# Kernel tuning notes

Measured on AMD Instinct MI355X. Metric: run time of the kernel, lower is better.

## Reference

```python
import jax, jax.numpy as jnp
import numpy as np

NUM_DIRECTIONS = 100  # matches init_kwargs
N_POINTS = 200000


def setup_inputs() -> dict:
    key = jax.random.key(0)
    k1, k2 = jax.random.split(key)
    X = jax.random.normal(k1, (N_POINTS, 2), dtype=jnp.float32)
    Y = jax.random.normal(k2, (N_POINTS, 2), dtype=jnp.float32)
    return {"X": X, "Y": Y}


def _lines():
    # thetas = linspace(-pi/2, pi/2, K+1)[:-1]; lines[i] = (cos t_i, sin t_i)
    thetas = jnp.linspace(-np.pi / 2, np.pi / 2, NUM_DIRECTIONS + 1)[:-1]
    L = jnp.stack([jnp.cos(thetas), jnp.sin(thetas)], axis=1).astype(jnp.float32)  # [K, 2]
    return L


def reference(X, Y):
    # X, Y: [N, 2], [M, 2] persistence diagrams (birth, death)
    L = _lines()                                   # [K, 2]
    inv_norm = 1.0 / jnp.sum(L * L, axis=1)        # [K] (== 1 analytically, kept for fidelity)
    diag = jnp.array([0.5, 0.5], dtype=jnp.float32)

    # diagonal projections of each diagram: sum(point) * [0.5, 0.5]
    X_diag = jnp.sum(X, axis=1, keepdims=True) * diag  # [N, 2]
    Y_diag = jnp.sum(Y, axis=1, keepdims=True) * diag  # [M, 2]

    # batched line projections: replaces per-point dot-product loops
    proj_X = (X @ L.T) * inv_norm                  # [N, K]
    proj_Y = (Y @ L.T) * inv_norm                  # [M, K]
    proj_Xd = (X_diag @ L.T) * inv_norm            # [N, K]
    proj_Yd = (Y_diag @ L.T) * inv_norm            # [M, K]

    # 1D EMD per direction: sort both multisets, sum |diff|
    A = jnp.sort(jnp.concatenate([proj_X, proj_Yd], axis=0), axis=0)  # [N+M, K]
    B = jnp.sort(jnp.concatenate([proj_Y, proj_Xd], axis=0), axis=0)  # [N+M, K]

    total_cost = jnp.sum(jnp.abs(A - B)) / NUM_DIRECTIONS
    return total_cost
```

## Files before the change

### kernel.cpp

```cpp
#include <hip/hip_runtime.h>

#define KDIR 100
#define TILE 4096
#define NPASS 3
#define MBLK 512
#define MOUT 4096
#define MPT 8

struct TrueT  { static constexpr bool value = true; };
struct FalseT { static constexpr bool value = false; };

__device__ __forceinline__ unsigned encodeF(float f) {
  unsigned u = __float_as_uint(f);
  return u ^ ((u >> 31) ? 0xFFFFFFFFu : 0x80000000u);
}
__device__ __forceinline__ float decodeU(unsigned u) {
  return __uint_as_float(u ^ ((u >> 31) ? 0x80000000u : 0xFFFFFFFFu));
}

__global__ void k_table(float* tbl, double* part, int nSlots) {
  int k = threadIdx.x;
  const double PI = 3.14159265358979323846;
  if (k < KDIR) {
    double th = -PI * 0.5 + (double)k * (PI / (double)KDIR);
    float c = (float)cos(th), s = (float)sin(th);
    float invn = 1.0f / (c * c + s * s);
    tbl[k] = c; tbl[128 + k] = s; tbl[256 + k] = (c + s) * invn; tbl[384 + k] = invn;
  }
  if (k == 100) { tbl[100] = 0.5f; tbl[228] = 0.5f; tbl[484] = 1.0f; }
  for (int i = k; i < nSlots; i += 256) part[i] = 0.0;
}

__device__ __forceinline__ void buildTile(const float* __restrict__ p0, int nItems,
                                          float ck, float sk, float inv,
                                          unsigned* __restrict__ d0, unsigned* h, int tid) {
  if (nItems == TILE) {
    const float4* p4 = (const float4*)p0;
    uint2* o2 = (uint2*)d0;
#pragma unroll
    for (int i = 0; i < 8; ++i) {
      float4 v = p4[i * 256 + tid];
      unsigned ua = encodeF((v.x * ck + v.y * sk) * inv);
      unsigned ub = encodeF((v.z * ck + v.w * sk) * inv);
      o2[i * 256 + tid] = make_uint2(ua, ub);
      atomicAdd(&h[(ua >> 8) & 255u], 1u);
      atomicAdd(&h[(ub >> 8) & 255u], 1u);
    }
  } else {
    for (int j = tid; j < nItems; j += 256) {
      float x = p0[2 * j], y = p0[2 * j + 1];
      unsigned u = encodeF((x * ck + y * sk) * inv);
      d0[j] = u;
      atomicAdd(&h[(u >> 8) & 255u], 1u);
    }
  }
}

__global__ __launch_bounds__(256) void k_buildAll(const float* __restrict__ X,
                                                  const float* __restrict__ Y, int n,
                                                  const float* __restrict__ tbl,
                                                  unsigned* __restrict__ dst,
                                                  unsigned* __restrict__ counts, int T) {
  __shared__ unsigned h[256];
  int tid = threadIdx.x;
  h[tid] = 0;
  __syncthreads();
  int dir = blockIdx.y;
  int k = (dir < KDIR) ? dir : (dir < 2 * KDIR ? dir - KDIR : KDIR);
  const float* P = (dir < KDIR || dir == 2 * KDIR) ? X : Y;
  float ck = tbl[k], sk = tbl[128 + k], inv = tbl[384 + k];
  int tile = blockIdx.x;
  int start = tile * TILE;
  int nItems = min(TILE, n - start);
  buildTile(P + 2 * (size_t)start, nItems, ck, sk, inv,
            dst + (size_t)dir * n + start, h, tid);
  __syncthreads();
  counts[((size_t)dir * 256 + tid) * T + tile] = h[tid];
}

__global__ __launch_bounds__(256) void k_build(const float* __restrict__ P, int n, int kIdx,
                                               const float* __restrict__ tbl,
                                               unsigned* __restrict__ dst,
                                               unsigned* __restrict__ counts, int T, int seg0) {
  __shared__ unsigned h[256];
  int tid = threadIdx.x;
  h[tid] = 0;
  __syncthreads();
  int dir = blockIdx.y;
  int k = kIdx + dir;
  float ck = tbl[k], sk = tbl[128 + k], inv = tbl[384 + k];
  int tile = blockIdx.x;
  int start = tile * TILE;
  int nItems = min(TILE, n - start);
  buildTile(P + 2 * (size_t)start, nItems, ck, sk, inv,
            dst + (size_t)dir * n + start, h, tid);
  __syncthreads();
  counts[((size_t)(seg0 + dir) * 256 + tid) * T + tile] = h[tid];
}

__global__ __launch_bounds__(256) void k_hist8(const unsigned* __restrict__ keys,
                                               int L, int T, int shift,
                                               unsigned* __restrict__ counts) {
  __shared__ unsigned h[4][256];
  int tid = threadIdx.x;
  int w = tid >> 6;
  for (int i = tid; i < 4 * 256; i += 256) ((unsigned*)h)[i] = 0;
  __syncthreads();
  int seg = blockIdx.y, tile = blockIdx.x;
  const unsigned* base = keys + (size_t)seg * L + (size_t)tile * TILE;
  int nItems = min(TILE, L - tile * TILE);
  if (nItems == TILE) {
    const uint4* b4 = (const uint4*)base;
#pragma unroll
    for (int i = 0; i < 4; ++i) {
      uint4 v = b4[i * 256 + tid];
      atomicAdd(&h[w][(v.x >> shift) & 255u], 1u);
      atomicAdd(&h[w][(v.y >> shift) & 255u], 1u);
      atomicAdd(&h[w][(v.z >> shift) & 255u], 1u);
      atomicAdd(&h[w][(v.w >> shift) & 255u], 1u);
    }
  } else {
    for (int i = tid; i < nItems; i += 256)
      atomicAdd(&h[w][(base[i] >> shift) & 255u], 1u);
  }
  __syncthreads();
  counts[((size_t)seg * 256 + tid) * T + tile] =
      h[0][tid] + h[1][tid] + h[2][tid] + h[3][tid];
}

__global__ __launch_bounds__(256) void k_scanSeg(unsigned* __restrict__ counts, int T) {
  __shared__ unsigned tot[256];
  unsigned* c = counts + (size_t)blockIdx.x * 256 * T;
  int tid = threadIdx.x;
  int base = tid * T;
  unsigned sum = 0;
  for (int i = 0; i < T; ++i) sum += c[base + i];
  tot[tid] = sum;
  __syncthreads();
  for (int ofs = 1; ofs < 256; ofs <<= 1) {
    unsigned t = (tid >= ofs) ? tot[tid - ofs] : 0u;
    __syncthreads();
    tot[tid] += t;
    __syncthreads();
  }
  unsigned run = tot[tid] - sum;
  for (int i = 0; i < T; ++i) {
    unsigned v = c[base + i];
    c[base + i] = run;
    run += v;
  }
}

__global__ __launch_bounds__(256) void k_scatter8(const unsigned* __restrict__ src,
                                                  unsigned* __restrict__ dst,
                                                  int L, int T, int shift,
                                                  const unsigned* __restrict__ counts,
                                                  unsigned* __restrict__ nextCounts,
                                                  int shift2) {
  __shared__ unsigned runG[4][4][256];
  __shared__ unsigned diffD[256];
  __shared__ unsigned wsum[4];
  int tid = threadIdx.x;
  int lane = tid & 63, w = tid >> 6;
  int seg = blockIdx.y, tile = blockIdx.x;
  const unsigned* sbase = src + (size_t)seg * L + (size_t)tile * TILE;
  int nItems = min(TILE, L - tile * TILE);
  for (int i = tid; i < 4 * 4 * 256; i += 256) ((unsigned*)runG)[i] = 0;
  __syncthreads();
  unsigned kk[16];
  unsigned rr[16];
  unsigned long long laneLT = (1ull << lane) - 1ull;
  unsigned long long aboveM = ~((laneLT << 1) | 1ull);
  int jbase = w * (TILE / 4);

  auto body = [&](auto FULLC) {
    constexpr bool FULL = decltype(FULLC)::value;
#pragma unroll
    for (int i = 0; i < 16; ++i) {
      int j = jbase + i * 64 + lane;
      kk[i] = (FULL || j < nItems) ? sbase[j] : 0xFFFFFFFFu;
    }
#pragma unroll
    for (int s = 0; s < 4; ++s) {
      unsigned long long mask[4];
      unsigned prev[4];
#pragma unroll
      for (int g = 0; g < 4; ++g) {
        int i = g * 4 + s;
        unsigned d = (kk[i] >> shift) & 255u;
        unsigned long long m = FULL ? ~0ull : __ballot(jbase + i * 64 + lane < nItems);
#pragma unroll
        for (int b = 0; b < 8; ++b) {
          unsigned long long bal = __ballot((d >> b) & 1);
          m &= ((d >> b) & 1) ? bal : ~bal;
        }
        mask[g] = m;
        prev[g] = runG[w][g][d];
      }
#pragma unroll
      for (int g = 0; g < 4; ++g) {
        int i = g * 4 + s;
        if (FULL || jbase + i * 64 + lane < nItems) {
          unsigned d = (kk[i] >> shift) & 255u;
          unsigned r = (unsigned)__popcll(mask[g] & laneLT);
          rr[i] = prev[g] + r;
          if (r == 0) runG[w][g][d] = prev[g] + (unsigned)__popcll(mask[g]);
        }
      }
    }
    __syncthreads();
    {
      unsigned v[16];
#pragma unroll
      for (int w2 = 0; w2 < 4; ++w2)
#pragma unroll
        for (int g2 = 0; g2 < 4; ++g2) v[w2 * 4 + g2] = runG[w2][g2][tid];
      unsigned tot = 0;
#pragma unroll
      for (int i = 0; i < 16; ++i) {
        unsigned t = v[i];
        v[i] = tot;
        tot += t;
      }
      unsigned x = tot;
#pragma unroll
      for (int ofs = 1; ofs < 64; ofs <<= 1) {
        unsigned t = __shfl_up(x, ofs, 64);
        if (lane >= ofs) x += t;
      }
      if (lane == 63) wsum[w] = x;
      __syncthreads();
      unsigned basew = 0;
#pragma unroll
      for (int w2 = 0; w2 < 4; ++w2) basew += (w2 < w) ? wsum[w2] : 0u;
      unsigned localStart = basew + x - tot;
      diffD[tid] = counts[((size_t)seg * 256 + tid) * T + tile] - localStart;
#pragma unroll
      for (int w2 = 0; w2 < 4; ++w2)
#pragma unroll
        for (int g2 = 0; g2 < 4; ++g2)
          runG[w2][g2][tid] = v[w2 * 4 + g2] + localStart;
    }
    __syncthreads();
    unsigned lp[16];
#pragma unroll
    for (int i = 0; i < 16; ++i) {
      unsigned d = (kk[i] >> shift) & 255u;
      lp[i] = runG[w][i >> 2][d] + rr[i];
    }
    __syncthreads();
    unsigned* kbuf = &runG[0][0][0];
#pragma unroll
    for (int i = 0; i < 16; ++i) {
      if (FULL || jbase + i * 64 + lane < nItems) kbuf[lp[i]] = kk[i];
    }
    __syncthreads();
    unsigned* dbase = dst + (size_t)seg * L;
#pragma unroll
    for (int i = 0; i < 16; ++i) {
      int pos = i * 256 + tid;
      bool valid = FULL || pos < nItems;
      unsigned k = 0, g = 0, d2 = 0;
      if (valid) {
        k = kbuf[pos];
        unsigned d = (k >> shift) & 255u;
        g = diffD[d] + (unsigned)pos;
        dbase[g] = k;
        d2 = (k >> shift2) & 255u;
      }
      if (nextCounts) {
        unsigned pid = ((g >> 12) << 8) | d2;
        unsigned prevPid = __shfl_up(pid, 1, 64);
        bool leader = valid && (lane == 0 || pid != prevPid);
        unsigned long long lm = __ballot(leader);
        unsigned long long bounds;
        if (FULL) bounds = lm;
        else bounds = lm | ~__ballot(valid);
        if (leader) {
          unsigned long long above = bounds & aboveM;
          int nxt = above ? __builtin_ctzll(above) : 64;
          atomicAdd(&nextCounts[((size_t)seg * 256 + d2) * T + (g >> 12)],
                    (unsigned)(nxt - lane));
        }
      }
    }
  };
  if (nItems == TILE) body(TrueT{});
  else body(FalseT{});
}

__device__ __forceinline__ float scaledAt(const unsigned* __restrict__ s, int len, int j,
                                          float c, int rev) {
  return c * decodeU(s[rev ? (len - 1 - j) : j]);
}

__device__ int mergeSplit(const unsigned* __restrict__ U, int n,
                          const unsigned* __restrict__ sV, int m,
                          float c, int rev, int o) {
  int lo = o - m; if (lo < 0) lo = 0;
  int hi = o < n ? o : n;
  while (lo < hi) {
    int mid = (lo + hi + 1) >> 1;
    if (decodeU(U[mid - 1]) <= scaledAt(sV, m, o - mid, c, rev)) lo = mid;
    else hi = mid - 1;
  }
  return lo;
}

__global__ void k_splits(const unsigned* __restrict__ pX, const unsigned* __restrict__ pY,
                         const unsigned* __restrict__ sx, const unsigned* __restrict__ sy,
                         int N, int M, int k0, int mB,
                         const float* __restrict__ tbl, int* __restrict__ splits) {
  int b = blockIdx.x * blockDim.x + threadIdx.x;
  if (b >= mB) return;
  int kl = blockIdx.y;
  int kc = gridDim.y;
  float c = tbl[256 + k0 + kl];
  int rev = c < 0.0f ? 1 : 0;
  int Stot = N + M;
  int o = b * MOUT; if (o > Stot) o = Stot;
  const unsigned* U1 = pX + (size_t)kl * N;
  const unsigned* U2 = pY + (size_t)kl * M;
  splits[(size_t)kl * mB + b] = mergeSplit(U1, N, sy, M, c, rev, o);
  splits[((size_t)kc + kl) * mB + b] = mergeSplit(U2, M, sx, N, c, rev, o);
}

__device__ __forceinline__ int ldsSplit(const float* __restrict__ sArr, int aCnt, int bCnt,
                                        int o) {
  int lo = o - bCnt; if (lo < 0) lo = 0;
  int hi = o < aCnt ? o : aCnt;
  while (lo < hi) {
    int mid = (lo + hi + 1) >> 1;
    if (sArr[mid - 1] <= sArr[aCnt + o - mid]) lo = mid;
    else hi = mid - 1;
  }
  return lo;
}

__device__ __forceinline__ void merge8(const float* __restrict__ sArr, int aCnt, int bCnt,
                                       int la, int lb, float* m) {
  const float FMAX = 3.402823466e38f;
  float a[8], b[8];
#pragma unroll
  for (int j = 0; j < 8; ++j) {
    a[j] = (la + j < aCnt) ? sArr[la + j] : FMAX;
    b[j] = (lb + j < bCnt) ? sArr[aCnt + lb + j] : FMAX;
  }
#pragma unroll
  for (int j = 0; j < 8; ++j) m[j] = fminf(a[j], b[7 - j]);
#pragma unroll
  for (int d = 4; d > 0; d >>= 1) {
#pragma unroll
    for (int i = 0; i < 8; ++i) {
      if ((i & d) == 0 && (i | d) < 8) {
        float lo = fminf(m[i], m[i | d]);
        float hi = fmaxf(m[i], m[i | d]);
        m[i] = lo; m[i | d] = hi;
      }
    }
  }
}

__global__ __launch_bounds__(MBLK) void k_merge(const unsigned* __restrict__ pX,
                                                const unsigned* __restrict__ pY,
                                                const unsigned* __restrict__ sx,
                                                const unsigned* __restrict__ sy,
                                                int N, int M, int k0,
                                                const float* __restrict__ tbl,
                                                const int* __restrict__ splits, int mB,
                                                double* __restrict__ part) {
  __shared__ float sA[MOUT];
  __shared__ float sB[MOUT];
  __shared__ float red[MBLK];
  int kl = blockIdx.y;
  int kc = gridDim.y;
  float c = tbl[256 + k0 + kl];
  int rev = c < 0.0f ? 1 : 0;
  int Stot = N + M;
  int o0 = blockIdx.x * MOUT;
  int outCnt = min(MOUT, Stot - o0);
  const unsigned* U1 = pX + (size_t)kl * N;
  const unsigned* U2 = pY + (size_t)kl * M;
  int tid = threadIdx.x;
  int aLo = splits[(size_t)kl * mB + blockIdx.x];
  int aHi = splits[(size_t)kl * mB + blockIdx.x + 1];
  int a2Lo = splits[((size_t)kc + kl) * mB + blockIdx.x];
  int a2Hi = splits[((size_t)kc + kl) * mB + blockIdx.x + 1];
  int aCnt = aHi - aLo;
  int bLo = o0 - aLo, bCnt = outCnt - aCnt;
  int a2Cnt = a2Hi - a2Lo;
  int b2Lo = o0 - a2Lo, b2Cnt = outCnt - a2Cnt;
  for (int i = tid; i < aCnt; i += MBLK) sA[i] = decodeU(U1[aLo + i]);
  for (int i = tid; i < bCnt; i += MBLK) {
    int j = bLo + i;
    sA[aCnt + i] = c * decodeU(sy[rev ? (M - 1 - j) : j]);
  }
  for (int i = tid; i < a2Cnt; i += MBLK) sB[i] = decodeU(U2[a2Lo + i]);
  for (int i = tid; i < b2Cnt; i += MBLK) {
    int j = b2Lo + i;
    sB[a2Cnt + i] = c * decodeU(sx[rev ? (N - 1 - j) : j]);
  }
  __syncthreads();
  float acc = 0.0f;
  int lo0 = tid * MPT;
  if (lo0 < outCnt) {
    int cnt = min(MPT, outCnt - lo0);
    int la = ldsSplit(sA, aCnt, bCnt, lo0);
    int lb = lo0 - la;
    int la2 = ldsSplit(sB, a2Cnt, b2Cnt, lo0);
    int lb2 = lo0 - la2;
    float mA[8], mB2[8];
    merge8(sA, aCnt, bCnt, la, lb, mA);
    merge8(sB, a2Cnt, b2Cnt, la2, lb2, mB2);
#pragma unroll
    for (int j = 0; j < 8; ++j)
      if (j < cnt) acc += fabsf(mA[j] - mB2[j]);
  }
  red[tid] = acc;
  __syncthreads();
  for (int ofs = MBLK / 2; ofs > 0; ofs >>= 1) {
    if (tid < ofs) red[tid] += red[tid + ofs];
    __syncthreads();
  }
  if (tid == 0) {
    size_t slot = (size_t)(k0 + kl) * gridDim.x + blockIdx.x;
    part[slot] += (double)red[0];
  }
}

__global__ __launch_bounds__(256) void k_final(const double* __restrict__ part, int nSlots,
                                               float* __restrict__ out) {
  __shared__ double red[256];
  int tid = threadIdx.x;
  double s = 0.0;
  for (int i = tid; i < nSlots; i += 256) s += part[i];
  red[tid] = s;
  __syncthreads();
  for (int ofs = 128; ofs > 0; ofs >>= 1) {
    if (tid < ofs) red[tid] += red[tid + ofs];
    __syncthreads();
  }
  if (tid == 0) out[0] = (float)(red[0] / (double)KDIR);
}

extern "C" void kernel_launch(void* const* d_in, const int* in_sizes, int n_in,
                              void* d_out, int out_size, void* d_ws, size_t ws_size,
                              hipStream_t stream) {
  const float* X = (const float*)d_in[0];
  const float* Y = (const float*)d_in[1];
  int N = in_sizes[0] / 2;
  int M = in_sizes[1] / 2;

  char* ws = (char*)d_ws;
  size_t off = 0;
  auto alloc = [&](size_t b) -> void* {
    void* p = ws + off;
    off += (b + 255) & ~(size_t)255;
    return p;
  };
  float* tbl = (float*)alloc(512 * sizeof(float));
  unsigned* sPing = (unsigned*)alloc((size_t)(N + M) * 4);
  unsigned* sPong = (unsigned*)alloc((size_t)(N + M) * 4);

  int Tn = (N + TILE - 1) / TILE;
  int Tm = (M + TILE - 1) / TILE;
  int Tmax = Tn > Tm ? Tn : Tm;
  int mx = N > M ? N : M;
  int mBlocksAll = (N + M + MOUT - 1) / MOUT;
  int mB = mBlocksAll + 1;
  int nSlots = KDIR * mBlocksAll;
  int* splits = (int*)alloc((size_t)2 * KDIR * mB * 4);
  double* part = (double*)alloc((size_t)nSlots * 8);

  size_t perDir = (size_t)(N + M) * 8 + (size_t)4 * 256 * Tmax * 4;
  size_t reserve = (size_t)2 * mx * 8 + (size_t)4 * 256 * Tmax * 4;
  size_t remain = ws_size > off ? ws_size - off : 0;
  remain = remain > reserve ? remain - reserve : 0;
  int Kc = (int)(remain / perDir);
  if (Kc > KDIR) Kc = KDIR;
  if (Kc < 1) Kc = 1;
  int maxSegs = 2 * Kc + 2;
  size_t cntElems = (size_t)maxSegs * 256 * Tmax;
  unsigned* countsA = (unsigned*)alloc(cntElems * 4);
  unsigned* countsB = (unsigned*)alloc(cntElems * 4);
  unsigned* cPing = (unsigned*)alloc(((size_t)Kc * (N + M) + 2 * (size_t)mx) * 4);
  unsigned* cPong = (unsigned*)alloc(((size_t)Kc * (N + M) + 2 * (size_t)mx) * 4);

  k_table<<<1, 256, 0, stream>>>(tbl, part, nSlots);

  auto sortJob = [&](unsigned* ping, unsigned* pong, int segs, int L) {
    int T = (L + TILE - 1) / TILE;
    unsigned* s = pong;
    unsigned* d = ping;
    for (int p = 0; p < NPASS; ++p) {
      int shift = 8 * (p + 1);
      if (p > 0)
        k_hist8<<<dim3(T, segs), 256, 0, stream>>>(s, L, T, shift, countsA);
      k_scanSeg<<<segs, 256, 0, stream>>>(countsA, T);
      k_scatter8<<<dim3(T, segs), 256, 0, stream>>>(s, d, L, T, shift, countsA,
                                                    (unsigned*)nullptr, 0);
      unsigned* t = s; s = d; d = t;
    }
  };

  bool fused = (N == M) && (Kc == KDIR);

  if (fused) {
    int segs = 2 * KDIR + 2;
    int T = Tn;
    size_t cntBytes = (size_t)segs * 256 * T * 4;
    k_buildAll<<<dim3(Tn, segs), 256, 0, stream>>>(X, Y, N, tbl, cPong, countsA, T);
    hipMemsetAsync(countsB, 0, cntBytes, stream);
    k_scanSeg<<<segs, 256, 0, stream>>>(countsA, T);
    k_scatter8<<<dim3(T, segs), 256, 0, stream>>>(cPong, cPing, N, T, 8, countsA,
                                                  countsB, 16);
    k_scanSeg<<<segs, 256, 0, stream>>>(countsB, T);
    hipMemsetAsync(countsA, 0, cntBytes, stream);
    k_scatter8<<<dim3(T, segs), 256, 0, stream>>>(cPing, cPong, N, T, 16, countsB,
                                                  countsA, 24);
    k_scanSeg<<<segs, 256, 0, stream>>>(countsA, T);
    k_scatter8<<<dim3(T, segs), 256, 0, stream>>>(cPong, cPing, N, T, 24, countsA,
                                                  (unsigned*)nullptr, 0);
    unsigned* pX = cPing;
    unsigned* pY = cPing + (size_t)KDIR * N;
    unsigned* dX = cPing + (size_t)2 * KDIR * N;
    unsigned* dY = dX + N;
    k_splits<<<dim3((mB + 255) / 256, KDIR), 256, 0, stream>>>(pX, pY, dX, dY, N, M, 0, mB,
                                                               tbl, splits);
    k_merge<<<dim3(mBlocksAll, KDIR), MBLK, 0, stream>>>(pX, pY, dX, dY, N, M, 0, tbl,
                                                         splits, mB, part);
  } else {
    if (N == M) {
      k_build<<<dim3(Tn, 1), 256, 0, stream>>>(X, N, 100, tbl, sPong, countsA, Tn, 0);
      k_build<<<dim3(Tn, 1), 256, 0, stream>>>(Y, N, 100, tbl, sPong + N, countsA, Tn, 1);
      sortJob(sPing, sPong, 2, N);
    } else {
      k_build<<<dim3(Tn, 1), 256, 0, stream>>>(X, N, 100, tbl, sPong, countsA, Tn, 0);
      sortJob(sPing, sPong, 1, N);
      k_build<<<dim3(Tm, 1), 256, 0, stream>>>(Y, M, 100, tbl, sPong + N, countsA, Tm, 0);
      sortJob(sPing + N, sPong + N, 1, M);
    }
    for (int k0 = 0; k0 < KDIR; k0 += Kc) {
      int kc = (KDIR - k0 < Kc) ? (KDIR - k0) : Kc;
      unsigned* pXin = cPong;
      unsigned* pYin = cPong + (size_t)kc * N;
      unsigned* pX = cPing;
      unsigned* pY = cPing + (size_t)kc * N;
      if (N == M) {
        k_build<<<dim3(Tn, kc), 256, 0, stream>>>(X, N, k0, tbl, pXin, countsA, Tn, 0);
        k_build<<<dim3(Tn, kc), 256, 0, stream>>>(Y, N, k0, tbl, pYin, countsA, Tn, kc);
        sortJob(cPing, cPong, 2 * kc, N);
      } else {
        k_build<<<dim3(Tn, kc), 256, 0, stream>>>(X, N, k0, tbl, pXin, countsA, Tn, 0);
        sortJob(pX, pXin, kc, N);
        k_build<<<dim3(Tm, kc), 256, 0, stream>>>(Y, M, k0, tbl, pYin, countsA, Tm, 0);
        sortJob(pY, pYin, kc, M);
      }
      k_splits<<<dim3((mB + 255) / 256, kc), 256, 0, stream>>>(pX, pY, sPing, sPing + N,
                                                               N, M, k0, mB, tbl, splits);
      k_merge<<<dim3(mBlocksAll, kc), MBLK, 0, stream>>>(pX, pY, sPing, sPing + N, N, M, k0,
                                                         tbl, splits, mB, part);
    }
  }
  k_final<<<1, 256, 0, stream>>>(part, nSlots, (float*)d_out);
}
```

Baseline: 911.9 us.

## Transpose radix count layout to tile-major and use per-wave build histograms

Changes the radix-sort digit count array from digit-major [seg][digit][tile] to tile-major [seg][tile][digit] in every kernel that writes or reads it. The build kernels, scan, scatter, and the atomic next-count updates all use the new indexing, so a block's 256 per-digit counts are written contiguously and the scan walks them with coalesced strided loads instead of each thread reading its own long row. The build kernels also switch to four per-wave shared histograms that are summed at the end, to cut LDS atomic contention. The cost is a little more shared memory and the extra reduction of the four histograms.

New measurement: 801.1 us. -12.1%, faster.

```diff
diff --git a/kernel.cpp b/kernel.cpp
--- a/kernel.cpp
+++ b/kernel.cpp
@@ -17,6 +17,7 @@
 __device__ __forceinline__ float decodeU(unsigned u) {
   return __uint_as_float(u ^ ((u >> 31) ? 0x80000000u : 0xFFFFFFFFu));
 }
+
 
 __global__ void k_table(float* tbl, double* part, int nSlots) {
   int k = threadIdx.x;
@@ -33,7 +34,9 @@
 
 __device__ __forceinline__ void buildTile(const float* __restrict__ p0, int nItems,
                                           float ck, float sk, float inv,
-                                          unsigned* __restrict__ d0, unsigned* h, int tid) {
+                                          unsigned* __restrict__ d0,
+                                          unsigned (*h)[256], int tid) {
+  int w = tid >> 6;
   if (nItems == TILE) {
     const float4* p4 = (const float4*)p0;
     uint2* o2 = (uint2*)d0;
@@ -43,15 +46,15 @@
       unsigned ua = encodeF((v.x * ck + v.y * sk) * inv);
       unsigned ub = encodeF((v.z * ck + v.w * sk) * inv);
       o2[i * 256 + tid] = make_uint2(ua, ub);
-      atomicAdd(&h[(ua >> 8) & 255u], 1u);
-      atomicAdd(&h[(ub >> 8) & 255u], 1u);
+      atomicAdd(&h[w][(ua >> 8) & 255u], 1u);
+      atomicAdd(&h[w][(ub >> 8) & 255u], 1u);
     }
   } else {
     for (int j = tid; j < nItems; j += 256) {
       float x = p0[2 * j], y = p0[2 * j + 1];
       unsigned u = encodeF((x * ck + y * sk) * inv);
       d0[j] = u;
-      atomicAdd(&h[(u >> 8) & 255u], 1u);
+      atomicAdd(&h[w][(u >> 8) & 255u], 1u);
     }
   }
 }
@@ -61,9 +64,9 @@
                                                   const float* __restrict__ tbl,
                                                   unsigned* __restrict__ dst,
                                                   unsigned* __restrict__ counts, int T) {
-  __shared__ unsigned h[256];
-  int tid = threadIdx.x;
-  h[tid] = 0;
+  __shared__ unsigned h[4][256];
+  int tid = threadIdx.x;
+  for (int i = tid; i < 4 * 256; i += 256) ((unsigned*)h)[i] = 0;
   __syncthreads();
   int dir = blockIdx.y;
   int k = (dir < KDIR) ? dir : (dir < 2 * KDIR ? dir - KDIR : KDIR);
@@ -75,16 +78,17 @@
   buildTile(P + 2 * (size_t)start, nItems, ck, sk, inv,
             dst + (size_t)dir * n + start, h, tid);
   __syncthreads();
-  counts[((size_t)dir * 256 + tid) * T + tile] = h[tid];
+  counts[((size_t)dir * T + tile) * 256 + tid] =
+      h[0][tid] + h[1][tid] + h[2][tid] + h[3][tid];
 }
 
 __global__ __launch_bounds__(256) void k_build(const float* __restrict__ P, int n, int kIdx,
                                                const float* __restrict__ tbl,
                                                unsigned* __restrict__ dst,
                                                unsigned* __restrict__ counts, int T, int seg0) {
-  __shared__ unsigned h[256];
-  int tid = threadIdx.x;
-  h[tid] = 0;
+  __shared__ unsigned h[4][256];
+  int tid = threadIdx.x;
+  for (int i = tid; i < 4 * 256; i += 256) ((unsigned*)h)[i] = 0;
   __syncthreads();
   int dir = blockIdx.y;
   int k = kIdx + dir;
@@ -95,7 +99,8 @@
   buildTile(P + 2 * (size_t)start, nItems, ck, sk, inv,
             dst + (size_t)dir * n + start, h, tid);
   __syncthreads();
-  counts[((size_t)(seg0 + dir) * 256 + tid) * T + tile] = h[tid];
+  counts[((size_t)(seg0 + dir) * T + tile) * 256 + tid] =
+      h[0][tid] + h[1][tid] + h[2][tid] + h[3][tid];
 }
 
 __global__ __launch_bounds__(256) void k_hist8(const unsigned* __restrict__ keys,
@@ -124,7 +129,7 @@
       atomicAdd(&h[w][(base[i] >> shift) & 255u], 1u);
   }
   __syncthreads();
-  counts[((size_t)seg * 256 + tid) * T + tile] =
+  counts[((size_t)seg * T + tile) * 256 + tid] =
       h[0][tid] + h[1][tid] + h[2][tid] + h[3][tid];
 }
 
@@ -132,9 +137,8 @@
   __shared__ unsigned tot[256];
   unsigned* c = counts + (size_t)blockIdx.x * 256 * T;
   int tid = threadIdx.x;
-  int base = tid * T;
   unsigned sum = 0;
-  for (int i = 0; i < T; ++i) sum += c[base + i];
+  for (int i = 0; i < T; ++i) sum += c[i * 256 + tid];
   tot[tid] = sum;
   __syncthreads();
   for (int ofs = 1; ofs < 256; ofs <<= 1) {
@@ -145,8 +149,8 @@
   }
   unsigned run = tot[tid] - sum;
   for (int i = 0; i < T; ++i) {
-    unsigned v = c[base + i];
-    c[base + i] = run;
+    unsigned v = c[i * 256 + tid];
+    c[i * 256 + tid] = run;
     run += v;
   }
 }
@@ -234,7 +238,7 @@
 #pragma unroll
       for (int w2 = 0; w2 < 4; ++w2) basew += (w2 < w) ? wsum[w2] : 0u;
       unsigned localStart = basew + x - tot;
-      diffD[tid] = counts[((size_t)seg * 256 + tid) * T + tile] - localStart;
+      diffD[tid] = counts[((size_t)seg * T + tile) * 256 + tid] - localStart;
 #pragma unroll
       for (int w2 = 0; w2 < 4; ++w2)
 #pragma unroll
@@ -279,7 +283,7 @@
         if (leader) {
           unsigned long long above = bounds & aboveM;
           int nxt = above ? __builtin_ctzll(above) : 64;
-          atomicAdd(&nextCounts[((size_t)seg * 256 + d2) * T + (g >> 12)],
+          atomicAdd(&nextCounts[((size_t)seg * T + (g >> 12)) * 256 + d2],
                     (unsigned)(nxt - lane));
         }
       }
```
